# Performance work log

Hardware: AMD Instinct MI355X
Metric: run time of the kernel (lower is better)

The kernel has to match this reference:

```python
import jax, jax.numpy as jnp
import numpy as np

NTIME = 20      # number of time blocks
V = 128         # vehicle_num per time block
F_OUT = 128     # out_features (== in_features here)
ALPHA = 0.2     # LeakyReLU negative slope
NEG = -9e15     # mask fill value used by the torch module


def setup_inputs() -> dict:
    key = jax.random.key(0)
    k1, k2, k3, k4 = jax.random.split(key, 4)
    h = jax.random.normal(k1, (NTIME * V, F_OUT), dtype=jnp.float32)
    # binary adjacency mask, broadcast over the feature dim like the torch code
    adj = jax.random.randint(k2, (V, V, 1), 0, 2).astype(jnp.float32)
    share_weight = jax.random.normal(k3, (F_OUT, F_OUT), dtype=jnp.float32) * 0.05
    a = jax.random.normal(k4, (2 * F_OUT, F_OUT), dtype=jnp.float32) * 0.05
    return {"h": h, "adj": adj, "share_weight": share_weight, "a": a}


def reference(h, adj, share_weight, a):
    # Wh: [N, F]
    Wh = h @ share_weight
    # a_input @ a decomposes: e[p,q,:] = leakyrelu(Wh[p] @ a[:F] + Wh[q] @ a[F:])
    # Only the block-diagonal (per-time) slices of e are ever used, so compute
    # blocks directly instead of the full NxNxF tensor.
    a1, a2 = a[:F_OUT], a[F_OUT:]
    e1 = (Wh @ a1).reshape(NTIME, V, F_OUT)  # [T, v, F]
    e2 = (Wh @ a2).reshape(NTIME, V, F_OUT)
    e = e1[:, :, None, :] + e2[:, None, :, :]           # [T, v, v, F]
    e = jnp.where(e > 0, e, ALPHA * e)                   # LeakyReLU
    masked = jnp.where(adj[None] > 0, e, NEG)            # mask per time block
    # torch softmax(dim=1) on [v, v, F] blocks -> axis=2 here (the j index)
    attention_raw = jax.nn.softmax(masked, axis=2)       # [T, v, v, F]
    # training=False => dropout is identity.
    # h_prime[t,b,f] = sum_j att[t,b,j,f] * Wh[t,j,f]  (the diagonal-of-matmul trick)
    Whb = Wh.reshape(NTIME, V, F_OUT)
    h_prime = jnp.einsum('tbjf,tjf->tbf', attention_raw, Whb)
    out = jax.nn.elu(h_prime)                            # concat=True branch
    return (out, attention_raw)
```

## Files before the change

kernel.cpp:

```cpp
#include <hip/hip_runtime.h>
#include <hip/hip_bf16.h>
#include <math.h>

#define NTIME 20
#define V 128
#define F 128
constexpr float ALPHA = 0.2f;

__global__ __launch_bounds__(128) void k_wa(const float* __restrict__ W,
                                            const float* __restrict__ a,
                                            float* __restrict__ Wa) {
  const int i = blockIdx.x;
  const int s = blockIdx.y;
  const int k = threadIdx.x;
  __shared__ float wrow[F];
  wrow[k] = W[i * F + k];
  __syncthreads();
  const float* as = a + s * F * F;
  float acc = 0.f;
#pragma unroll 8
  for (int m = 0; m < F; ++m) acc += wrow[m] * as[m * F + k];
  Wa[(s * F + i) * F + k] = acc;
}

__global__ __launch_bounds__(256) void k_gemm(const float* __restrict__ h,
                                              const float* __restrict__ W,
                                              const float* __restrict__ Wa,
                                              float* __restrict__ Wh,
                                              float* __restrict__ E1,
                                              float* __restrict__ E2) {
  __shared__ float Alds[64][129];
  __shared__ float Blds[128][64];
  const int tid = threadIdx.x;
  const int rb = blockIdx.x * 64;
  const int matc = blockIdx.y >> 1;
  const int cb = (blockIdx.y & 1) * 64;

#pragma unroll
  for (int p = 0; p < 8; ++p) {
    int id = tid + p * 256;
    int row = id >> 5;
    int c0 = (id & 31) * 4;
    float4 v = *reinterpret_cast<const float4*>(&h[(rb + row) * F + c0]);
    Alds[row][c0 + 0] = v.x; Alds[row][c0 + 1] = v.y;
    Alds[row][c0 + 2] = v.z; Alds[row][c0 + 3] = v.w;
  }
  const float* src = (matc == 0) ? W : (Wa + (matc - 1) * F * F);
#pragma unroll
  for (int p = 0; p < 8; ++p) {
    int id = tid + p * 256;
    int k = id >> 4;
    int c0 = (id & 15) * 4;
    float4 v = *reinterpret_cast<const float4*>(&src[k * F + cb + c0]);
    Blds[k][c0 + 0] = v.x; Blds[k][c0 + 1] = v.y;
    Blds[k][c0 + 2] = v.z; Blds[k][c0 + 3] = v.w;
  }
  __syncthreads();

  const int tx = tid & 15;
  const int ty = tid >> 4;
  float acc[4][4] = {};
#pragma unroll 4
  for (int k = 0; k < 128; ++k) {
    float4 bv = *reinterpret_cast<const float4*>(&Blds[k][tx * 4]);
    float a0 = Alds[ty * 4 + 0][k];
    float a1 = Alds[ty * 4 + 1][k];
    float a2 = Alds[ty * 4 + 2][k];
    float a3 = Alds[ty * 4 + 3][k];
    acc[0][0] += a0 * bv.x; acc[0][1] += a0 * bv.y; acc[0][2] += a0 * bv.z; acc[0][3] += a0 * bv.w;
    acc[1][0] += a1 * bv.x; acc[1][1] += a1 * bv.y; acc[1][2] += a1 * bv.z; acc[1][3] += a1 * bv.w;
    acc[2][0] += a2 * bv.x; acc[2][1] += a2 * bv.y; acc[2][2] += a2 * bv.z; acc[2][3] += a2 * bv.w;
    acc[3][0] += a3 * bv.x; acc[3][1] += a3 * bv.y; acc[3][2] += a3 * bv.z; acc[3][3] += a3 * bv.w;
  }

  float* Dp = (matc == 0) ? Wh : ((matc == 1) ? E1 : E2);
  const int gr0 = rb + ty * 4;
  const int c0 = cb + tx * 4;
#pragma unroll
  for (int i = 0; i < 4; ++i) {
    float4 v;
    v.x = acc[i][0]; v.y = acc[i][1]; v.z = acc[i][2]; v.w = acc[i][3];
    *reinterpret_cast<float4*>(&Dp[(gr0 + i) * F + c0]) = v;
  }
}

__global__ __launch_bounds__(256) void k_attn(const float* __restrict__ Wh,
                                              const float* __restrict__ E1,
                                              const float* __restrict__ E2,
                                              const float* __restrict__ adj,
                                              float* __restrict__ out,
                                              float* __restrict__ att) {
  __shared__ float sA[2][4][F];
  __shared__ float hA[2][4][F];
  __shared__ float invA[2][F];
  __shared__ float uniA[2];

  const int r0 = blockIdx.x * 2;
  const int r1 = r0 + 1;
  const int t = r0 >> 7;
  const int b0 = r0 & 127;
  const int w = threadIdx.x >> 6;
  const int lane = threadIdx.x & 63;
  const int fc = lane * 2;
  const int j0 = w * 32;

  const float* E2t = E2 + t * V * F;
  const float* Wht = Wh + t * V * F;
  const float* adj0 = adj + b0 * V;
  const float* adj1 = adj0 + V;

  const bool in32 = lane < 32;
  const unsigned long long Ma = __ballot(in32 ? (adj0[j0 + (lane & 31)] > 0.f) : false);
  const unsigned long long Mb = __ballot(in32 ? (adj1[j0 + (lane & 31)] > 0.f) : false);

  const float2 e1a = *reinterpret_cast<const float2*>(E1 + r0 * F + fc);
  const float2 e1b = *reinterpret_cast<const float2*>(E1 + r1 * F + fc);

  float sa0 = 0.f, sa1 = 0.f, ha0 = 0.f, ha1 = 0.f;
  float sb0 = 0.f, sb1 = 0.f, hb0 = 0.f, hb1 = 0.f;
#pragma unroll 4
  for (int jj = 0; jj < 32; ++jj) {
    const bool ta = (Ma >> jj) & 1;
    const bool tb = (Mb >> jj) & 1;
    if (ta | tb) {
      const int j = j0 + jj;
      float2 e2 = *reinterpret_cast<const float2*>(E2t + j * F + fc);
      float2 wv = *reinterpret_cast<const float2*>(Wht + j * F + fc);
      if (ta) {
        float x0 = e1a.x + e2.x, x1 = e1a.y + e2.y;
        x0 = x0 > 0.f ? x0 : ALPHA * x0;
        x1 = x1 > 0.f ? x1 : ALPHA * x1;
        float p0 = __expf(x0), p1 = __expf(x1);
        sa0 += p0; sa1 += p1; ha0 += p0 * wv.x; ha1 += p1 * wv.y;
      }
      if (tb) {
        float x0 = e1b.x + e2.x, x1 = e1b.y + e2.y;
        x0 = x0 > 0.f ? x0 : ALPHA * x0;
        x1 = x1 > 0.f ? x1 : ALPHA * x1;
        float p0 = __expf(x0), p1 = __expf(x1);
        sb0 += p0; sb1 += p1; hb0 += p0 * wv.x; hb1 += p1 * wv.y;
      }
    }
  }
  sA[0][w][fc] = sa0; sA[0][w][fc + 1] = sa1;
  hA[0][w][fc] = ha0; hA[0][w][fc + 1] = ha1;
  sA[1][w][fc] = sb0; sA[1][w][fc + 1] = sb1;
  hA[1][w][fc] = hb0; hA[1][w][fc + 1] = hb1;
  __syncthreads();

  if (w < 2) {
    const int row = w;
    const int r = r0 + row;
    const float S0 = sA[row][0][fc] + sA[row][1][fc] + sA[row][2][fc] + sA[row][3][fc];
    const float S1 = sA[row][0][fc + 1] + sA[row][1][fc + 1] + sA[row][2][fc + 1] + sA[row][3][fc + 1];
    const bool uni = (S0 == 0.f);
    const float inv0 = uni ? (1.f / (float)V) : (1.f / S0);
    const float inv1 = uni ? (1.f / (float)V) : (1.f / S1);
    invA[row][fc] = inv0; invA[row][fc + 1] = inv1;
    if (lane == 0) uniA[row] = uni ? 1.f : 0.f;

    float H0, H1;
    if (uni) {
      H0 = 0.f; H1 = 0.f;
      for (int j = 0; j < V; ++j) {
        float2 wv = *reinterpret_cast<const float2*>(Wht + j * F + fc);
        H0 += wv.x; H1 += wv.y;
      }
      H0 *= inv0; H1 *= inv1;
    } else {
      H0 = (hA[row][0][fc] + hA[row][1][fc] + hA[row][2][fc] + hA[row][3][fc]) * inv0;
      H1 = (hA[row][0][fc + 1] + hA[row][1][fc + 1] + hA[row][2][fc + 1] + hA[row][3][fc + 1]) * inv1;
    }
    float2 ov;
    ov.x = H0 > 0.f ? H0 : __expf(H0) - 1.f;
    ov.y = H1 > 0.f ? H1 : __expf(H1) - 1.f;
    *reinterpret_cast<float2*>(out + r * F + fc) = ov;
  }
  __syncthreads();

  const int jh = lane >> 5;
  const int f4 = (lane & 31) * 4;
  const float4 e1qa = *reinterpret_cast<const float4*>(E1 + r0 * F + f4);
  const float4 e1qb = *reinterpret_cast<const float4*>(E1 + r1 * F + f4);
  const float4 invqa = *reinterpret_cast<const float4*>(&invA[0][f4]);
  const float4 invqb = *reinterpret_cast<const float4*>(&invA[1][f4]);
  const bool ua = uniA[0] != 0.f;
  const bool ub = uniA[1] != 0.f;
  float* attb0 = att + (size_t)r0 * (V * F);
  float* attb1 = att + (size_t)r1 * (V * F);

#pragma unroll 4
  for (int jj = 0; jj < 16; ++jj) {
    const int j = j0 + jj * 2 + jh;
    const float4 e2q = *reinterpret_cast<const float4*>(E2t + j * F + f4);
    const float ga = (adj0[j] > 0.f) ? 1.f : 0.f;
    const float gb = (adj1[j] > 0.f) ? 1.f : 0.f;

    {
      float x0 = e1qa.x + e2q.x, x1 = e1qa.y + e2q.y;
      float x2 = e1qa.z + e2q.z, x3 = e1qa.w + e2q.w;
      x0 = x0 > 0.f ? x0 : ALPHA * x0;
      x1 = x1 > 0.f ? x1 : ALPHA * x1;
      x2 = x2 > 0.f ? x2 : ALPHA * x2;
      x3 = x3 > 0.f ? x3 : ALPHA * x3;
      float4 o;
      o.x = __expf(x0) * invqa.x * ga;
      o.y = __expf(x1) * invqa.y * ga;
      o.z = __expf(x2) * invqa.z * ga;
      o.w = __expf(x3) * invqa.w * ga;
      if (ua) { o.x = invqa.x; o.y = invqa.y; o.z = invqa.z; o.w = invqa.w; }
      *reinterpret_cast<float4*>(attb0 + j * F + f4) = o;
    }
    {
      float x0 = e1qb.x + e2q.x, x1 = e1qb.y + e2q.y;
      float x2 = e1qb.z + e2q.z, x3 = e1qb.w + e2q.w;
      x0 = x0 > 0.f ? x0 : ALPHA * x0;
      x1 = x1 > 0.f ? x1 : ALPHA * x1;
      x2 = x2 > 0.f ? x2 : ALPHA * x2;
      x3 = x3 > 0.f ? x3 : ALPHA * x3;
      float4 o;
      o.x = __expf(x0) * invqb.x * gb;
      o.y = __expf(x1) * invqb.y * gb;
      o.z = __expf(x2) * invqb.z * gb;
      o.w = __expf(x3) * invqb.w * gb;
      if (ub) { o.x = invqb.x; o.y = invqb.y; o.z = invqb.z; o.w = invqb.w; }
      *reinterpret_cast<float4*>(attb1 + j * F + f4) = o;
    }
  }
}

extern "C" void kernel_launch(void* const* d_in, const int* in_sizes, int n_in,
                              void* d_out, int out_size, void* d_ws, size_t ws_size,
                              hipStream_t stream) {
  (void)in_sizes; (void)n_in; (void)out_size; (void)ws_size;
  const float* h   = (const float*)d_in[0];
  const float* adj = (const float*)d_in[1];
  const float* W   = (const float*)d_in[2];
  const float* a   = (const float*)d_in[3];

  float* Wh = (float*)d_ws;
  float* E1 = Wh + NTIME * V * F;
  float* E2 = E1 + NTIME * V * F;
  float* Wa = E2 + NTIME * V * F;

  float* out = (float*)d_out;
  float* att = out + NTIME * V * F;

  k_wa<<<dim3(128, 2), 128, 0, stream>>>(W, a, Wa);
  k_gemm<<<dim3(40, 6), 256, 0, stream>>>(h, W, Wa, Wh, E1, E2);
  k_attn<<<dim3(NTIME * V / 2), 256, 0, stream>>>(Wh, E1, E2, adj, out, att);
}
```

Baseline: 199.7 us.

## Use nontemporal attention stores, branchless masking, smaller GEMM tiles, occupancy hint

The attention write loop now reads mask bits from the ballot result instead of reloading adj, and it takes a fast path with nontemporal vector stores when neither row is fully masked. The row-reduction loop drops its branches and multiplies by a 0/1 mask, and it uses fmaxf for the LeakyReLU. The GEMM tile shrinks to 32 rows, which doubles the block count for better CU coverage, and k_attn gets an occupancy hint in its launch bounds. The goal is to cut write-cache pollution and divergence in the large attention-tensor store. In exchange, masked entries now cost wasted exp work, and the shift of a 32-bit mask by up to 31 must stay in range.

```diff
diff --git a/kernel.cpp b/kernel.cpp
--- a/kernel.cpp
+++ b/kernel.cpp
@@ -1,11 +1,12 @@
 #include <hip/hip_runtime.h>
-#include <hip/hip_bf16.h>
 #include <math.h>
 
 #define NTIME 20
 #define V 128
 #define F 128
 constexpr float ALPHA = 0.2f;
+
+typedef float f32x4 __attribute__((ext_vector_type(4)));
 
 __global__ __launch_bounds__(128) void k_wa(const float* __restrict__ W,
                                             const float* __restrict__ a,
@@ -29,15 +30,15 @@
                                               float* __restrict__ Wh,
                                               float* __restrict__ E1,
                                               float* __restrict__ E2) {
-  __shared__ float Alds[64][129];
+  __shared__ float Alds[32][129];
   __shared__ float Blds[128][64];
   const int tid = threadIdx.x;
-  const int rb = blockIdx.x * 64;
+  const int rb = blockIdx.x * 32;
   const int matc = blockIdx.y >> 1;
   const int cb = (blockIdx.y & 1) * 64;
 
 #pragma unroll
-  for (int p = 0; p < 8; ++p) {
+  for (int p = 0; p < 4; ++p) {
     int id = tid + p * 256;
     int row = id >> 5;
     int c0 = (id & 31) * 4;
@@ -59,37 +60,33 @@
 
   const int tx = tid & 15;
   const int ty = tid >> 4;
-  float acc[4][4] = {};
+  float acc[2][4] = {};
 #pragma unroll 4
   for (int k = 0; k < 128; ++k) {
     float4 bv = *reinterpret_cast<const float4*>(&Blds[k][tx * 4]);
-    float a0 = Alds[ty * 4 + 0][k];
-    float a1 = Alds[ty * 4 + 1][k];
-    float a2 = Alds[ty * 4 + 2][k];
-    float a3 = Alds[ty * 4 + 3][k];
+    float a0 = Alds[ty * 2 + 0][k];
+    float a1 = Alds[ty * 2 + 1][k];
     acc[0][0] += a0 * bv.x; acc[0][1] += a0 * bv.y; acc[0][2] += a0 * bv.z; acc[0][3] += a0 * bv.w;
     acc[1][0] += a1 * bv.x; acc[1][1] += a1 * bv.y; acc[1][2] += a1 * bv.z; acc[1][3] += a1 * bv.w;
-    acc[2][0] += a2 * bv.x; acc[2][1] += a2 * bv.y; acc[2][2] += a2 * bv.z; acc[2][3] += a2 * bv.w;
-    acc[3][0] += a3 * bv.x; acc[3][1] += a3 * bv.y; acc[3][2] += a3 * bv.z; acc[3][3] += a3 * bv.w;
   }
 
   float* Dp = (matc == 0) ? Wh : ((matc == 1) ? E1 : E2);
-  const int gr0 = rb + ty * 4;
+  const int gr0 = rb + ty * 2;
   const int c0 = cb + tx * 4;
 #pragma unroll
-  for (int i = 0; i < 4; ++i) {
+  for (int i = 0; i < 2; ++i) {
     float4 v;
     v.x = acc[i][0]; v.y = acc[i][1]; v.z = acc[i][2]; v.w = acc[i][3];
     *reinterpret_cast<float4*>(&Dp[(gr0 + i) * F + c0]) = v;
   }
 }
 
-__global__ __launch_bounds__(256) void k_attn(const float* __restrict__ Wh,
-                                              const float* __restrict__ E1,
-                                              const float* __restrict__ E2,
-                                              const float* __restrict__ adj,
-                                              float* __restrict__ out,
-                                              float* __restrict__ att) {
+__global__ __launch_bounds__(256, 5) void k_attn(const float* __restrict__ Wh,
+                                                 const float* __restrict__ E1,
+                                                 const float* __restrict__ E2,
+                                                 const float* __restrict__ adj,
+                                                 float* __restrict__ out,
+                                                 float* __restrict__ att) {
   __shared__ float sA[2][4][F];
   __shared__ float hA[2][4][F];
   __shared__ float invA[2][F];
@@ -112,35 +109,33 @@
   const bool in32 = lane < 32;
   const unsigned long long Ma = __ballot(in32 ? (adj0[j0 + (lane & 31)] > 0.f) : false);
   const unsigned long long Mb = __ballot(in32 ? (adj1[j0 + (lane & 31)] > 0.f) : false);
+  const unsigned ma32 = (unsigned)Ma;
+  const unsigned mb32 = (unsigned)Mb;
 
   const float2 e1a = *reinterpret_cast<const float2*>(E1 + r0 * F + fc);
   const float2 e1b = *reinterpret_cast<const float2*>(E1 + r1 * F + fc);
 
   float sa0 = 0.f, sa1 = 0.f, ha0 = 0.f, ha1 = 0.f;
   float sb0 = 0.f, sb1 = 0.f, hb0 = 0.f, hb1 = 0.f;
-#pragma unroll 4
+#pragma unroll 8
   for (int jj = 0; jj < 32; ++jj) {
-    const bool ta = (Ma >> jj) & 1;
-    const bool tb = (Mb >> jj) & 1;
-    if (ta | tb) {
-      const int j = j0 + jj;
-      float2 e2 = *reinterpret_cast<const float2*>(E2t + j * F + fc);
-      float2 wv = *reinterpret_cast<const float2*>(Wht + j * F + fc);
-      if (ta) {
-        float x0 = e1a.x + e2.x, x1 = e1a.y + e2.y;
-        x0 = x0 > 0.f ? x0 : ALPHA * x0;
-        x1 = x1 > 0.f ? x1 : ALPHA * x1;
-        float p0 = __expf(x0), p1 = __expf(x1);
-        sa0 += p0; sa1 += p1; ha0 += p0 * wv.x; ha1 += p1 * wv.y;
-      }
-      if (tb) {
-        float x0 = e1b.x + e2.x, x1 = e1b.y + e2.y;
-        x0 = x0 > 0.f ? x0 : ALPHA * x0;
-        x1 = x1 > 0.f ? x1 : ALPHA * x1;
-        float p0 = __expf(x0), p1 = __expf(x1);
-        sb0 += p0; sb1 += p1; hb0 += p0 * wv.x; hb1 += p1 * wv.y;
-      }
-    }
+    const int j = j0 + jj;
+    const float2 e2 = *reinterpret_cast<const float2*>(E2t + j * F + fc);
+    const float2 wv = *reinterpret_cast<const float2*>(Wht + j * F + fc);
+    const float ga = (float)((ma32 >> jj) & 1u);
+    const float gb = (float)((mb32 >> jj) & 1u);
+    float x0 = e1a.x + e2.x, x1 = e1a.y + e2.y;
+    x0 = fmaxf(x0, ALPHA * x0);
+    x1 = fmaxf(x1, ALPHA * x1);
+    float p0 = __expf(x0) * ga, p1 = __expf(x1) * ga;
+    sa0 += p0; sa1 += p1;
+    ha0 = fmaf(p0, wv.x, ha0); ha1 = fmaf(p1, wv.y, ha1);
+    x0 = e1b.x + e2.x; x1 = e1b.y + e2.y;
+    x0 = fmaxf(x0, ALPHA * x0);
+    x1 = fmaxf(x1, ALPHA * x1);
+    p0 = __expf(x0) * gb; p1 = __expf(x1) * gb;
+    sb0 += p0; sb1 += p1;
+    hb0 = fmaf(p0, wv.x, hb0); hb1 = fmaf(p1, wv.y, hb1);
   }
   sA[0][w][fc] = sa0; sA[0][w][fc + 1] = sa1;
   hA[0][w][fc] = ha0; hA[0][w][fc + 1] = ha1;
@@ -188,43 +183,65 @@
   const bool ub = uniA[1] != 0.f;
   float* attb0 = att + (size_t)r0 * (V * F);
   float* attb1 = att + (size_t)r1 * (V * F);
-
+  const unsigned maL = ma32 >> jh;
+  const unsigned mbL = mb32 >> jh;
+
+  if (!(ua | ub)) {
 #pragma unroll 4
-  for (int jj = 0; jj < 16; ++jj) {
-    const int j = j0 + jj * 2 + jh;
-    const float4 e2q = *reinterpret_cast<const float4*>(E2t + j * F + f4);
-    const float ga = (adj0[j] > 0.f) ? 1.f : 0.f;
-    const float gb = (adj1[j] > 0.f) ? 1.f : 0.f;
-
-    {
+    for (int jj = 0; jj < 16; ++jj) {
+      const int j = j0 + jj * 2 + jh;
+      const float4 e2q = *reinterpret_cast<const float4*>(E2t + j * F + f4);
+      const float ga = (float)((maL >> (2 * jj)) & 1u);
+      const float gb = (float)((mbL >> (2 * jj)) & 1u);
+      const float va0 = invqa.x * ga, va1 = invqa.y * ga, va2 = invqa.z * ga, va3 = invqa.w * ga;
+      const float vb0 = invqb.x * gb, vb1 = invqb.y * gb, vb2 = invqb.z * gb, vb3 = invqb.w * gb;
+
       float x0 = e1qa.x + e2q.x, x1 = e1qa.y + e2q.y;
       float x2 = e1qa.z + e2q.z, x3 = e1qa.w + e2q.w;
-      x0 = x0 > 0.f ? x0 : ALPHA * x0;
-      x1 = x1 > 0.f ? x1 : ALPHA * x1;
-      x2 = x2 > 0.f ? x2 : ALPHA * x2;
-      x3 = x3 > 0.f ? x3 : ALPHA * x3;
-      float4 o;
-      o.x = __expf(x0) * invqa.x * ga;
-      o.y = __expf(x1) * invqa.y * ga;
-      o.z = __expf(x2) * invqa.z * ga;
-      o.w = __expf(x3) * invqa.w * ga;
-      if (ua) { o.x = invqa.x; o.y = invqa.y; o.z = invqa.z; o.w = invqa.w; }
-      *reinterpret_cast<float4*>(attb0 + j * F + f4) = o;
+      x0 = fmaxf(x0, ALPHA * x0); x1 = fmaxf(x1, ALPHA * x1);
+      x2 = fmaxf(x2, ALPHA * x2); x3 = fmaxf(x3, ALPHA * x3);
+      f32x4 o;
+      o.x = __expf(x0) * va0; o.y = __expf(x1) * va1;
+      o.z = __expf(x2) * va2; o.w = __expf(x3) * va3;
+      __builtin_nontemporal_store(o, reinterpret_cast<f32x4*>(attb0 + j * F + f4));
+
+      x0 = e1qb.x + e2q.x; x1 = e1qb.y + e2q.y;
+      x2 = e1qb.z + e2q.z; x3 = e1qb.w + e2q.w;
+      x0 = fmaxf(x0, ALPHA * x0); x1 = fmaxf(x1, ALPHA * x1);
+      x2 = fmaxf(x2, ALPHA * x2); x3 = fmaxf(x3, ALPHA * x3);
+      o.x = __expf(x0) * vb0; o.y = __expf(x1) * vb1;
+      o.z = __expf(x2) * vb2; o.w = __expf(x3) * vb3;
+      __builtin_nontemporal_store(o, reinterpret_cast<f32x4*>(attb1 + j * F + f4));
     }
-    {
-      float x0 = e1qb.x + e2q.x, x1 = e1qb.y + e2q.y;
-      float x2 = e1qb.z + e2q.z, x3 = e1qb.w + e2q.w;
-      x0 = x0 > 0.f ? x0 : ALPHA * x0;
-      x1 = x1 > 0.f ? x1 : ALPHA * x1;
-      x2 = x2 > 0.f ? x2 : ALPHA * x2;
-      x3 = x3 > 0.f ? x3 : ALPHA * x3;
-      float4 o;
-      o.x = __expf(x0) * invqb.x * gb;
-      o.y = __expf(x1) * invqb.y * gb;
-      o.z = __expf(x2) * invqb.z * gb;
-      o.w = __expf(x3) * invqb.w * gb;
-      if (ub) { o.x = invqb.x; o.y = invqb.y; o.z = invqb.z; o.w = invqb.w; }
-      *reinterpret_cast<float4*>(attb1 + j * F + f4) = o;
+  } else {
+#pragma unroll 2
+    for (int jj = 0; jj < 16; ++jj) {
+      const int j = j0 + jj * 2 + jh;
+      const float4 e2q = *reinterpret_cast<const float4*>(E2t + j * F + f4);
+      const float ga = (float)((maL >> (2 * jj)) & 1u);
+      const float gb = (float)((mbL >> (2 * jj)) & 1u);
+      {
+        float x0 = e1qa.x + e2q.x, x1 = e1qa.y + e2q.y;
+        float x2 = e1qa.z + e2q.z, x3 = e1qa.w + e2q.w;
+        x0 = fmaxf(x0, ALPHA * x0); x1 = fmaxf(x1, ALPHA * x1);
+        x2 = fmaxf(x2, ALPHA * x2); x3 = fmaxf(x3, ALPHA * x3);
+        float4 o;
+        o.x = __expf(x0) * invqa.x * ga; o.y = __expf(x1) * invqa.y * ga;
+        o.z = __expf(x2) * invqa.z * ga; o.w = __expf(x3) * invqa.w * ga;
+        if (ua) { o.x = invqa.x; o.y = invqa.y; o.z = invqa.z; o.w = invqa.w; }
+        *reinterpret_cast<float4*>(attb0 + j * F + f4) = o;
+      }
+      {
+        float x0 = e1qb.x + e2q.x, x1 = e1qb.y + e2q.y;
+        float x2 = e1qb.z + e2q.z, x3 = e1qb.w + e2q.w;
+        x0 = fmaxf(x0, ALPHA * x0); x1 = fmaxf(x1, ALPHA * x1);
+        x2 = fmaxf(x2, ALPHA * x2); x3 = fmaxf(x3, ALPHA * x3);
+        float4 o;
+        o.x = __expf(x0) * invqb.x * gb; o.y = __expf(x1) * invqb.y * gb;
+        o.z = __expf(x2) * invqb.z * gb; o.w = __expf(x3) * invqb.w * gb;
+        if (ub) { o.x = invqb.x; o.y = invqb.y; o.z = invqb.z; o.w = invqb.w; }
+        *reinterpret_cast<float4*>(attb1 + j * F + f4) = o;
+      }
     }
   }
 }
@@ -247,6 +264,6 @@
   float* att = out + NTIME * V * F;
 
   k_wa<<<dim3(128, 2), 128, 0, stream>>>(W, a, Wa);
-  k_gemm<<<dim3(40, 6), 256, 0, stream>>>(h, W, Wa, Wh, E1, E2);
+  k_gemm<<<dim3(80, 6), 256, 0, stream>>>(h, W, Wa, Wh, E1, E2);
   k_attn<<<dim3(NTIME * V / 2), 256, 0, stream>>>(Wh, E1, E2, adj, out, att);
 }
```

After: 199.3 us. No clear change (-0.2%).
